# Kernel optimization log

Hardware: AMD Instinct MI355X
Metric: run time of the kernel (lower is better)

Reference implementation:

```python
import jax, jax.numpy as jnp
import numpy as np

N, C, NUM_GROUPS = 4_194_304, 16, 8


def setup_inputs() -> dict:
    key = jax.random.key(0)
    k1, k2, k3 = jax.random.split(key, 3)
    input_ = jax.random.normal(k1, (N, C), dtype=jnp.float32)
    target = jax.random.randint(k2, (N,), 0, C, dtype=jnp.int64) if jax.config.jax_enable_x64 else jax.random.randint(k2, (N,), 0, C, dtype=jnp.int32)
    group = jax.random.randint(k3, (N,), 0, NUM_GROUPS, dtype=jnp.int32)
    return {"input_": input_, "target": target, "group": group}


def reference(input_, target, group):
    # gather input_[i, target[i]] and take |1 - .|
    err = jnp.abs(1.0 - jnp.take_along_axis(input_, target[:, None].astype(jnp.int32), axis=1)[:, 0])  # [N]
    # per-group mean == L1-row-normalized one-hot matmul in the original
    sums = jax.ops.segment_sum(err, group, num_segments=NUM_GROUPS)               # [G]
    counts = jax.ops.segment_sum(jnp.ones_like(err), group, num_segments=NUM_GROUPS)
    means = jnp.where(counts > 0, sums / jnp.maximum(counts, 1.0), 0.0)           # empty group -> 0 (F.normalize eps behavior)
    loss_target_value = 0.5
    return jnp.abs(loss_target_value - means.mean())
```

## Files before the change

### kernel.cpp

```cpp
#include <hip/hip_runtime.h>

#define N_ELEMS 4194304
#define C_DIM 16
#define G_NUM 8

#define BLOCKS 2048
#define TPB 256
#define NTHREADS (BLOCKS * TPB)
#define NCLIQUES (NTHREADS / 4)
#define ITERS (N_ELEMS / NCLIQUES)

typedef float vfloat4 __attribute__((ext_vector_type(4)));


__global__ __launch_bounds__(TPB) void berl_partial(
    const float* __restrict__ input_,
    const int*   __restrict__ target,
    const int*   __restrict__ group,
    float*       __restrict__ part)
{
    const int tid   = threadIdx.x;
    const int lane  = tid & 3;
    const int gcliq = (blockIdx.x * TPB + tid) >> 2;

    float sums[G_NUM];
    float cnts[G_NUM];
#pragma unroll
    for (int k = 0; k < G_NUM; ++k) { sums[k] = 0.0f; cnts[k] = 0.0f; }

    const vfloat4* in4 = (const vfloat4*)input_;

#pragma unroll 4
    for (int it = 0; it < ITERS; ++it) {
        const int row = gcliq + it * NCLIQUES;
        vfloat4 v = __builtin_nontemporal_load(&in4[row * 4 + lane]);
        const int t = target[row];
        const int g = group[row];

        const int e2 = t & 3;
        float x = v.x;
        x = (e2 == 1) ? v.y : x;
        x = (e2 == 2) ? v.z : x;
        x = (e2 == 3) ? v.w : x;

        const bool own = ((t >> 2) == lane);
        const float e  = own ? fabsf(1.0f - x) : 0.0f;
        const float c1 = own ? 1.0f : 0.0f;

#pragma unroll
        for (int k = 0; k < G_NUM; ++k) {
            sums[k] += (g == k) ? e  : 0.0f;
            cnts[k] += (g == k) ? c1 : 0.0f;
        }
    }

    __shared__ float s_sums[G_NUM];
    __shared__ float s_cnts[G_NUM];
    if (tid < G_NUM) { s_sums[tid] = 0.0f; s_cnts[tid] = 0.0f; }
    __syncthreads();
#pragma unroll
    for (int k = 0; k < G_NUM; ++k) {
        atomicAdd(&s_sums[k], sums[k]);
        atomicAdd(&s_cnts[k], cnts[k]);
    }
    __syncthreads();
    if (tid < G_NUM)            part[blockIdx.x * 16 + tid] = s_sums[tid];
    else if (tid < 2 * G_NUM)   part[blockIdx.x * 16 + tid] = s_cnts[tid - G_NUM];
}

__global__ __launch_bounds__(256) void berl_final(
    const float* __restrict__ part,
    float*       __restrict__ out)
{
    __shared__ float s_acc[256];
    __shared__ float s_tot[16];
    const int tid = threadIdx.x;
    const int j   = tid & 15;
    const int b0  = tid >> 4;

    float acc = 0.0f;
    for (int k = 0; k < BLOCKS / 16; ++k)
        acc += part[(b0 + 16 * k) * 16 + j];
    s_acc[tid] = acc;
    __syncthreads();

    if (tid < 16) {
        float tot = 0.0f;
#pragma unroll
        for (int r = 0; r < 16; ++r) tot += s_acc[r * 16 + tid];
        s_tot[tid] = tot;
    }
    __syncthreads();

    if (tid == 0) {
        float acc2 = 0.0f;
#pragma unroll
        for (int g = 0; g < G_NUM; ++g) {
            const float c = s_tot[8 + g];
            const float m = (c > 0.0f) ? (s_tot[g] / fmaxf(c, 1.0f)) : 0.0f;
            acc2 += m;
        }
        out[0] = fabsf(0.5f - acc2 / (float)G_NUM);
    }
}

extern "C" void kernel_launch(void* const* d_in, const int* in_sizes, int n_in,
                              void* d_out, int out_size, void* d_ws, size_t ws_size,
                              hipStream_t stream) {
    const float* input_ = (const float*)d_in[0];
    const int*   target = (const int*)d_in[1];
    const int*   group  = (const int*)d_in[2];
    float* out  = (float*)d_out;
    float* part = (float*)d_ws;

    dim3 block(TPB);
    dim3 grid(BLOCKS);
    berl_partial<<<grid, block, 0, stream>>>(input_, target, group, part);
    berl_final<<<1, 256, 0, stream>>>(part, out);
}
```

Measured before the change: 427.7 us.

## Gather only target elements instead of streaming full input rows

Replaces the four-lane cooperative float4 read of every input row with a per-thread loop that loads int4 vectors of target and group and directly gathers only the selected input element for four rows. This aims to cut the bytes fetched from the large input matrix, since only one float per 16-float row is needed. It also drops the redundant per-lane reads of target and group. The cost is uncoalesced scattered scalar loads whose efficiency depends on memory sector granularity, plus a grid-stride loop with a runtime stride.

```diff
diff --git a/kernel.cpp b/kernel.cpp
--- a/kernel.cpp
+++ b/kernel.cpp
@@ -6,11 +6,6 @@
 
 #define BLOCKS 2048
 #define TPB 256
-#define NTHREADS (BLOCKS * TPB)
-#define NCLIQUES (NTHREADS / 4)
-#define ITERS (N_ELEMS / NCLIQUES)
-
-typedef float vfloat4 __attribute__((ext_vector_type(4)));
 
 
 __global__ __launch_bounds__(TPB) void berl_partial(
@@ -19,38 +14,36 @@
     const int*   __restrict__ group,
     float*       __restrict__ part)
 {
-    const int tid   = threadIdx.x;
-    const int lane  = tid & 3;
-    const int gcliq = (blockIdx.x * TPB + tid) >> 2;
+    const int tid = threadIdx.x;
 
     float sums[G_NUM];
     float cnts[G_NUM];
 #pragma unroll
-    for (int k = 0; k < G_NUM; ++k) { sums[k] = 0.0f; cnts[k] = 0.0f; }
+    for (int g = 0; g < G_NUM; ++g) { sums[g] = 0.0f; cnts[g] = 0.0f; }
 
-    const vfloat4* in4 = (const vfloat4*)input_;
+    const int4* t4 = (const int4*)target;
+    const int4* g4 = (const int4*)group;
+    const int n4     = N_ELEMS / 4;
+    const int stride = gridDim.x * blockDim.x;
 
-#pragma unroll 4
-    for (int it = 0; it < ITERS; ++it) {
-        const int row = gcliq + it * NCLIQUES;
-        vfloat4 v = __builtin_nontemporal_load(&in4[row * 4 + lane]);
-        const int t = target[row];
-        const int g = group[row];
-
-        const int e2 = t & 3;
-        float x = v.x;
-        x = (e2 == 1) ? v.y : x;
-        x = (e2 == 2) ? v.z : x;
-        x = (e2 == 3) ? v.w : x;
-
-        const bool own = ((t >> 2) == lane);
-        const float e  = own ? fabsf(1.0f - x) : 0.0f;
-        const float c1 = own ? 1.0f : 0.0f;
-
+    for (int i = blockIdx.x * blockDim.x + tid; i < n4; i += stride) {
+        int4 t = t4[i];
+        int4 g = g4[i];
+        const int base = i * (4 * C_DIM);
+        float e0 = fabsf(1.0f - __builtin_nontemporal_load(&input_[base + 0 * C_DIM + t.x]));
+        float e1 = fabsf(1.0f - __builtin_nontemporal_load(&input_[base + 1 * C_DIM + t.y]));
+        float e2 = fabsf(1.0f - __builtin_nontemporal_load(&input_[base + 2 * C_DIM + t.z]));
+        float e3 = fabsf(1.0f - __builtin_nontemporal_load(&input_[base + 3 * C_DIM + t.w]));
 #pragma unroll
         for (int k = 0; k < G_NUM; ++k) {
-            sums[k] += (g == k) ? e  : 0.0f;
-            cnts[k] += (g == k) ? c1 : 0.0f;
+            sums[k] += (g.x == k) ? e0 : 0.0f;
+            sums[k] += (g.y == k) ? e1 : 0.0f;
+            sums[k] += (g.z == k) ? e2 : 0.0f;
+            sums[k] += (g.w == k) ? e3 : 0.0f;
+            cnts[k] += (g.x == k) ? 1.0f : 0.0f;
+            cnts[k] += (g.y == k) ? 1.0f : 0.0f;
+            cnts[k] += (g.z == k) ? 1.0f : 0.0f;
+            cnts[k] += (g.w == k) ? 1.0f : 0.0f;
         }
     }
 
@@ -64,6 +57,7 @@
         atomicAdd(&s_cnts[k], cnts[k]);
     }
     __syncthreads();
+
     if (tid < G_NUM)            part[blockIdx.x * 16 + tid] = s_sums[tid];
     else if (tid < 2 * G_NUM)   part[blockIdx.x * 16 + tid] = s_cnts[tid - G_NUM];
 }
```

Measured after the change: 408.5 us. -4.5%, faster.
